# Performance work log

Measured on AMD Instinct MI355X. Metric: run time of the kernel, lower is better.

Reference implementation:

```python
import jax, jax.numpy as jnp
import numpy as np
import math

B, H, S, D = 4, 8, 512, 64

def setup_inputs() -> dict:
    key = jax.random.key(0)
    k1, k2, k3, k4, k5 = jax.random.split(key, 5)
    return {
        "query": jax.random.normal(k1, (B, H, S, D), dtype=jnp.float32),
        "key": jax.random.normal(k2, (B, H, S, D), dtype=jnp.float32),
        "value": jax.random.normal(k3, (B, H, S, D), dtype=jnp.float32),
        "relem": jax.random.normal(k4, (B, S, S, D), dtype=jnp.float32),
        "mask": jax.random.randint(k5, (B, S), 0, 2, dtype=jnp.int32),
    }

def reference(query, key, value, relem, mask):
    d = query.shape[-1]
    # relscore[b,h,s,t] = sum_d q[b,h,s,d] * relem[b,s,t,d]
    relscore = jnp.einsum("bhsd,bstd->bhst", query, relem)
    scores = jnp.einsum("bhsd,bhtd->bhst", query, key)
    scores = (relscore + scores) / math.sqrt(d)
    # mask [B,S] -> [B,1,S,S] (broadcast of key mask over query positions)
    m = mask[:, None, None, :]  # repeat over query dim is a broadcast
    scores = jnp.where(m == 0, jnp.float32(-1e9), scores)
    p_attn = jax.nn.softmax(scores, axis=-1)
    ans1 = jnp.einsum("bhst,bhtd->bhsd", p_attn, value)
    ans2 = jnp.einsum("bhst,bstd->bhsd", p_attn, relem)
    return ans1 + ans2, p_attn
```

## Files before the change

### kernel.cpp

```cpp
#include <hip/hip_runtime.h>


typedef __attribute__((ext_vector_type(8))) short short8;
typedef __attribute__((ext_vector_type(4))) float f32x4;

#define MFMA16(a, b, c) __builtin_amdgcn_mfma_f32_16x16x32_bf16(a, b, c, 0, 0, 0)

__device__ __forceinline__ unsigned short f2bf(float x) {
  unsigned int u = __float_as_uint(x);
  u += 0x7fffu + ((u >> 16) & 1u);
  return (unsigned short)(u >> 16);
}
__device__ __forceinline__ float bf2f(unsigned int s) {
  return __uint_as_float(s << 16);
}
__device__ __forceinline__ short8 pack8(const float4& a, const float4& b) {
  short8 r;
  r[0] = (short)f2bf(a.x); r[1] = (short)f2bf(a.y);
  r[2] = (short)f2bf(a.z); r[3] = (short)f2bf(a.w);
  r[4] = (short)f2bf(b.x); r[5] = (short)f2bf(b.y);
  r[6] = (short)f2bf(b.z); r[7] = (short)f2bf(b.w);
  return r;
}
__device__ __forceinline__ int RLI(int t, int d) {
  return ((t << 6) | d) ^ ((((t & 7) ^ ((t >> 3) & 7))) << 3);
}
__device__ __forceinline__ int SBI(int h, int t) {
  return ((h << 9) | t) ^ ((h & 7) << 3);
}

template <bool WSK>
__global__ __launch_bounds__(256, 4)
void qk_mfma(const float* __restrict__ Q, const float* __restrict__ K,
             void* __restrict__ skout) {
  const int bh   = blockIdx.x >> 6;
  const int tile = blockIdx.x & 63;
  const int s0 = (tile >> 3) << 6;
  const int t0 = (tile & 7) << 6;
  const int w    = threadIdx.x >> 6;
  const int lane = threadIdx.x & 63;
  const int rrow = lane & 15;
  const int kg   = lane >> 4;

  const float* Qb = Q + ((size_t)bh << 15);
  const float* Kb = K + ((size_t)bh << 15);

  const float* qp = Qb + (((s0 + (w << 4) + rrow) << 6) + (kg << 3));
  const short8 a0 = pack8(*reinterpret_cast<const float4*>(qp),
                          *reinterpret_cast<const float4*>(qp + 4));
  const short8 a1 = pack8(*reinterpret_cast<const float4*>(qp + 32),
                          *reinterpret_cast<const float4*>(qp + 36));

  float4 b0, b1, b2, b3;
  {
    const float* kp = Kb + (((t0 + rrow) << 6) + (kg << 3));
    b0 = *reinterpret_cast<const float4*>(kp);
    b1 = *reinterpret_cast<const float4*>(kp + 4);
    b2 = *reinterpret_cast<const float4*>(kp + 32);
    b3 = *reinterpret_cast<const float4*>(kp + 36);
  }
#pragma unroll
  for (int nt = 0; nt < 4; ++nt) {
    const short8 bb0 = pack8(b0, b1);
    const short8 bb1 = pack8(b2, b3);
    if (nt < 3) {
      const float* kp = Kb + (((t0 + ((nt + 1) << 4) + rrow) << 6) + (kg << 3));
      b0 = *reinterpret_cast<const float4*>(kp);
      b1 = *reinterpret_cast<const float4*>(kp + 4);
      b2 = *reinterpret_cast<const float4*>(kp + 32);
      b3 = *reinterpret_cast<const float4*>(kp + 36);
    }
    f32x4 c = {0.0f, 0.0f, 0.0f, 0.0f};
    c = MFMA16(a0, bb0, c);
    c = MFMA16(a1, bb1, c);
    const int tcol = t0 + (nt << 4) + rrow;
    const int srow = s0 + (w << 4) + (kg << 2);
    if constexpr (WSK) {
      unsigned short* ob = (unsigned short*)skout + ((size_t)bh << 18);
#pragma unroll
      for (int r = 0; r < 4; ++r)
        ob[(size_t)(srow + r) * 512 + tcol] = f2bf(c[r]);
    } else {
      float* ob = (float*)skout + ((size_t)bh << 18);
#pragma unroll
      for (int r = 0; r < 4; ++r)
        ob[(size_t)(srow + r) * 512 + tcol] = c[r];
    }
  }
}

template <bool WSK>
__global__ __launch_bounds__(512, 4)
void attn_v8(const float* __restrict__ Q, const float* __restrict__ R,
             const int* __restrict__ Mk, float* __restrict__ ans,
             float* __restrict__ pout, const void* __restrict__ skin) {
  __shared__ __align__(16) unsigned short smem[8 * 512 + 512 * 64];
  __shared__ __align__(16) float Pp[4][8][16];
  unsigned short* Sb = smem;
  unsigned short* Rl = smem + 8 * 512;

  const int tid = threadIdx.x;
  const int b = blockIdx.x >> 9;
  const int s = blockIdx.x & 511;
  const int bh0 = b << 3;

  const float* Rg = R + ((size_t)((b << 9) + s) << 15);

  {
    const int d4 = tid & 15;
    const int tr = tid >> 4;
#pragma unroll
    for (int pg = 0; pg < 2; ++pg) {
      float4 tmp[8];
#pragma unroll
      for (int j = 0; j < 8; ++j) {
        const int t = (pg << 8) + (j << 5) + tr;
        tmp[j] = *reinterpret_cast<const float4*>(Rg + (t << 6) + (d4 << 2));
      }
#pragma unroll
      for (int j = 0; j < 8; ++j) {
        const int t = (pg << 8) + (j << 5) + tr;
        unsigned short* dst = &Rl[RLI(t, d4 << 2)];
        dst[0] = f2bf(tmp[j].x); dst[1] = f2bf(tmp[j].y);
        dst[2] = f2bf(tmp[j].z); dst[3] = f2bf(tmp[j].w);
      }
    }
  }
  __syncthreads();

  const int lane = tid & 63;
  const int w    = tid >> 6;
  const int nn   = lane & 15;
  const int kg   = lane >> 4;

  {
    const int hq = nn & 7;
    const float* Qg = Q + ((size_t)(((bh0 + hq) << 9) + s) << 6);
    const short8 aq0 = pack8(*reinterpret_cast<const float4*>(Qg + (kg << 3)),
                             *reinterpret_cast<const float4*>(Qg + (kg << 3) + 4));
    const short8 aq1 = pack8(*reinterpret_cast<const float4*>(Qg + 32 + (kg << 3)),
                             *reinterpret_cast<const float4*>(Qg + 36 + (kg << 3)));

#pragma unroll
    for (int i = 0; i < 4; ++i) {
      const int t0 = ((w << 2) + i) << 4;
      const short8 bb0 = *reinterpret_cast<const short8*>(&Rl[RLI(t0 + nn, kg << 3)]);
      const short8 bb1 = *reinterpret_cast<const short8*>(&Rl[RLI(t0 + nn, 32 + (kg << 3))]);
      f32x4 c = {0.0f, 0.0f, 0.0f, 0.0f};
      c = MFMA16(aq0, bb0, c);
      c = MFMA16(aq1, bb1, c);
      if (kg < 2) {
#pragma unroll
        for (int r = 0; r < 4; ++r)
          Sb[SBI((kg << 2) + r, t0 + nn)] = f2bf(c[r]);
      }
    }
  }
  __syncthreads();

  {
    const int h = w;
    float bias[8];
#pragma unroll
    for (int k = 0; k < 8; ++k)
      bias[k] = Mk[(b << 9) + lane + (k << 6)] ? 0.0f : -1.0e9f;

    float* po = pout + ((size_t)(bh0 + h) << 18) + ((size_t)s << 9);
    const unsigned short* skw =
        WSK ? (const unsigned short*)skin + ((size_t)(bh0 + h) << 18) + ((size_t)s << 9)
            : nullptr;
    const float* skf =
        WSK ? nullptr
            : (const float*)skin + ((size_t)(bh0 + h) << 18) + ((size_t)s << 9);

    float v[8];
#pragma unroll
    for (int k = 0; k < 8; ++k) {
      const int t = lane + (k << 6);
      const float skv = WSK ? bf2f((unsigned int)skw[t]) : skf[t];
      v[k] = (bf2f((unsigned int)Sb[SBI(h, t)]) + skv) * 0.125f + bias[k];
    }
    float m = v[0];
#pragma unroll
    for (int k = 1; k < 8; ++k) m = fmaxf(m, v[k]);
    m = fmaxf(m, __shfl_xor(m, 1));
    m = fmaxf(m, __shfl_xor(m, 2));
    m = fmaxf(m, __shfl_xor(m, 4));
    m = fmaxf(m, __shfl_xor(m, 8));
    m = fmaxf(m, __shfl_xor(m, 16));
    m = fmaxf(m, __shfl_xor(m, 32));

    float e[8], ss = 0.0f;
#pragma unroll
    for (int k = 0; k < 8; ++k) { e[k] = __expf(v[k] - m); ss += e[k]; }
    ss += __shfl_xor(ss, 1);
    ss += __shfl_xor(ss, 2);
    ss += __shfl_xor(ss, 4);
    ss += __shfl_xor(ss, 8);
    ss += __shfl_xor(ss, 16);
    ss += __shfl_xor(ss, 32);
    const float inv = 1.0f / ss;

#pragma unroll
    for (int k = 0; k < 8; ++k) {
      const float p = e[k] * inv;
      const int t = lane + (k << 6);
      po[t] = p;
      Sb[SBI(h, t)] = f2bf(p);
    }
  }
  __syncthreads();

  {
    const int dt = w & 3;
    const int kh = w >> 2;
    const int n0 = dt << 4;

    f32x4 acc = {0.0f, 0.0f, 0.0f, 0.0f};
#pragma unroll
    for (int k8 = 0; k8 < 8; ++k8) {
      const int tb = (((kh << 3) + k8) << 5) + (kg << 3);
      const short8 af = *reinterpret_cast<const short8*>(&Sb[SBI(nn, tb)]);
      short8 bf;
#pragma unroll
      for (int j = 0; j < 8; ++j)
        bf[j] = (short)Rl[RLI(tb + j, n0 + nn)];
      acc = MFMA16(af, bf, acc);
    }
    if (kh == 1 && kg < 2) {
#pragma unroll
      for (int r = 0; r < 4; ++r)
        Pp[dt][(kg << 2) + r][nn] = acc[r];
    }
    __syncthreads();
    if (kh == 0 && kg < 2) {
#pragma unroll
      for (int r = 0; r < 4; ++r) {
        const int h = (kg << 2) + r;
        ans[((size_t)(((bh0 + h) << 9) + s) << 6) + n0 + nn] =
            acc[r] + Pp[dt][h][nn];
      }
    }
  }
}

__global__ __launch_bounds__(512, 4)
void pv_mfma(const float* __restrict__ V, const float* __restrict__ pout,
             float* __restrict__ ans) {
  __shared__ __align__(16) unsigned short Vl[512 * 64];

  const int tid = threadIdx.x;
  const int bh = blockIdx.x >> 4;
  const int s0 = (blockIdx.x & 15) << 5;

  const float* Vg = V + ((size_t)bh << 15);
  {
    const int d4 = tid & 15;
    const int tr = tid >> 4;
#pragma unroll
    for (int pg = 0; pg < 2; ++pg) {
      float4 tmp[8];
#pragma unroll
      for (int j = 0; j < 8; ++j) {
        const int t = (pg << 8) + (j << 5) + tr;
        tmp[j] = *reinterpret_cast<const float4*>(Vg + (t << 6) + (d4 << 2));
      }
#pragma unroll
      for (int j = 0; j < 8; ++j) {
        const int t = (pg << 8) + (j << 5) + tr;
        unsigned short* dst = &Vl[RLI(t, d4 << 2)];
        dst[0] = f2bf(tmp[j].x); dst[1] = f2bf(tmp[j].y);
        dst[2] = f2bf(tmp[j].z); dst[3] = f2bf(tmp[j].w);
      }
    }
  }
  __syncthreads();

  const int lane = tid & 63;
  const int w    = tid >> 6;
  const int nn   = lane & 15;
  const int kg   = lane >> 4;
  const int rw   = w & 1;
  const int cq   = w >> 1;
  const int n0   = cq << 4;
  const int srow = s0 + (rw << 4) + nn;

  const float* Pg = pout + ((size_t)bh << 18) + ((size_t)srow << 9);

  f32x4 acc = {0.f, 0.f, 0.f, 0.f};

  float4 pa = *reinterpret_cast<const float4*>(Pg + (kg << 3));
  float4 pb = *reinterpret_cast<const float4*>(Pg + (kg << 3) + 4);
#pragma unroll
  for (int ks = 0; ks < 16; ++ks) {
    const short8 af = pack8(pa, pb);
    if (ks < 15) {
      pa = *reinterpret_cast<const float4*>(Pg + ((ks + 1) << 5) + (kg << 3));
      pb = *reinterpret_cast<const float4*>(Pg + ((ks + 1) << 5) + (kg << 3) + 4);
    }
    const int tb = (ks << 5) + (kg << 3);
    short8 bf;
#pragma unroll
    for (int j = 0; j < 8; ++j)
      bf[j] = (short)Vl[RLI(tb + j, n0 + nn)];
    acc = MFMA16(af, bf, acc);
  }

  {
    const int sb = s0 + (rw << 4) + (kg << 2);
#pragma unroll
    for (int r = 0; r < 4; ++r) {
      float* ap = ans + ((size_t)bh << 15) + ((size_t)(sb + r) << 6) + n0 + nn;
      ap[0] += acc[r];
    }
  }
}

extern "C" void kernel_launch(void* const* d_in, const int* in_sizes, int n_in,
                              void* d_out, int out_size, void* d_ws, size_t ws_size,
                              hipStream_t stream) {
  const float* Q  = (const float*)d_in[0];
  const float* K  = (const float*)d_in[1];
  const float* V  = (const float*)d_in[2];
  const float* R  = (const float*)d_in[3];
  const int*   Mk = (const int*)d_in[4];
  float* ans  = (float*)d_out;
  float* pout = ans + (size_t)4 * 8 * 512 * 64;
  (void)in_sizes; (void)n_in; (void)out_size;

  const size_t sk_bf16_bytes = (size_t)4 * 8 * 512 * 512 * 2;

  if (ws_size >= sk_bf16_bytes) {
    hipLaunchKernelGGL((qk_mfma<true>), dim3(2048), dim3(256), 0, stream,
                       Q, K, d_ws);
    hipLaunchKernelGGL((attn_v8<true>), dim3(2048), dim3(512), 0, stream,
                       Q, R, Mk, ans, pout, d_ws);
  } else {
    hipLaunchKernelGGL((qk_mfma<false>), dim3(2048), dim3(256), 0, stream,
                       Q, K, pout);
    hipLaunchKernelGGL((attn_v8<false>), dim3(2048), dim3(512), 0, stream,
                       Q, R, Mk, ans, pout, pout);
  }
  hipLaunchKernelGGL(pv_mfma, dim3(512), dim3(512), 0, stream, V, pout, ans);
}
```

Before: 111.5 us.

## Pipeline relem staging with relscore MFMA and store QK scores as bf16 in pout

The relem tile load is split into two halves. The second half's global loads are issued before the first half's relscore MFMAs and converted into LDS afterwards, so load latency overlaps compute. The QK scores kernel now always writes bf16 values into the first half of each pout float row instead of into workspace, and attn_v10 prefetches those scores and the mask into registers before the relscore phase. This removes the workspace and fallback branch but adds an extra barrier and relies on each block reading its score row before it overwrites pout.

After: 106.1 us. -4.9%, faster.

```diff
diff --git a/kernel.cpp b/kernel.cpp
--- a/kernel.cpp
+++ b/kernel.cpp
@@ -29,10 +29,9 @@
   return ((h << 9) | t) ^ ((h & 7) << 3);
 }
 
-template <bool WSK>
 __global__ __launch_bounds__(256, 4)
 void qk_mfma(const float* __restrict__ Q, const float* __restrict__ K,
-             void* __restrict__ skout) {
+             float* __restrict__ pout) {
   const int bh   = blockIdx.x >> 6;
   const int tile = blockIdx.x & 63;
   const int s0 = (tile >> 3) << 6;
@@ -50,6 +49,8 @@
                           *reinterpret_cast<const float4*>(qp + 4));
   const short8 a1 = pack8(*reinterpret_cast<const float4*>(qp + 32),
                           *reinterpret_cast<const float4*>(qp + 36));
+
+  float* pb = pout + ((size_t)bh << 18);
 
   float4 b0, b1, b2, b3;
   {
@@ -75,25 +76,19 @@
     c = MFMA16(a1, bb1, c);
     const int tcol = t0 + (nt << 4) + rrow;
     const int srow = s0 + (w << 4) + (kg << 2);
-    if constexpr (WSK) {
-      unsigned short* ob = (unsigned short*)skout + ((size_t)bh << 18);
-#pragma unroll
-      for (int r = 0; r < 4; ++r)
-        ob[(size_t)(srow + r) * 512 + tcol] = f2bf(c[r]);
-    } else {
-      float* ob = (float*)skout + ((size_t)bh << 18);
-#pragma unroll
-      for (int r = 0; r < 4; ++r)
-        ob[(size_t)(srow + r) * 512 + tcol] = c[r];
-    }
-  }
-}
-
-template <bool WSK>
+#pragma unroll
+    for (int r = 0; r < 4; ++r) {
+      unsigned short* ob =
+          reinterpret_cast<unsigned short*>(pb + ((size_t)(srow + r) << 9));
+      ob[tcol] = f2bf(c[r]);
+    }
+  }
+}
+
 __global__ __launch_bounds__(512, 4)
-void attn_v8(const float* __restrict__ Q, const float* __restrict__ R,
-             const int* __restrict__ Mk, float* __restrict__ ans,
-             float* __restrict__ pout, const void* __restrict__ skin) {
+void attn_v10(const float* __restrict__ Q, const float* __restrict__ R,
+              const int* __restrict__ Mk, float* __restrict__ ans,
+              float* __restrict__ pout) {
   __shared__ __align__(16) unsigned short smem[8 * 512 + 512 * 64];
   __shared__ __align__(16) float Pp[4][8][16];
   unsigned short* Sb = smem;
@@ -106,26 +101,25 @@
 
   const float* Rg = R + ((size_t)((b << 9) + s) << 15);
 
-  {
-    const int d4 = tid & 15;
-    const int tr = tid >> 4;
-#pragma unroll
-    for (int pg = 0; pg < 2; ++pg) {
-      float4 tmp[8];
-#pragma unroll
-      for (int j = 0; j < 8; ++j) {
-        const int t = (pg << 8) + (j << 5) + tr;
-        tmp[j] = *reinterpret_cast<const float4*>(Rg + (t << 6) + (d4 << 2));
-      }
-#pragma unroll
-      for (int j = 0; j < 8; ++j) {
-        const int t = (pg << 8) + (j << 5) + tr;
-        unsigned short* dst = &Rl[RLI(t, d4 << 2)];
-        dst[0] = f2bf(tmp[j].x); dst[1] = f2bf(tmp[j].y);
-        dst[2] = f2bf(tmp[j].z); dst[3] = f2bf(tmp[j].w);
-      }
-    }
-  }
+  const int d4 = tid & 15;
+  const int tr = tid >> 4;
+
+  float4 buf[8];
+#pragma unroll
+  for (int j = 0; j < 8; ++j)
+    buf[j] = *reinterpret_cast<const float4*>(
+        Rg + (((j << 5) + tr) << 6) + (d4 << 2));
+#pragma unroll
+  for (int j = 0; j < 8; ++j) {
+    const int t = (j << 5) + tr;
+    unsigned short* dst = &Rl[RLI(t, d4 << 2)];
+    dst[0] = f2bf(buf[j].x); dst[1] = f2bf(buf[j].y);
+    dst[2] = f2bf(buf[j].z); dst[3] = f2bf(buf[j].w);
+  }
+#pragma unroll
+  for (int j = 0; j < 8; ++j)
+    buf[j] = *reinterpret_cast<const float4*>(
+        Rg + ((256 + (j << 5) + tr) << 6) + (d4 << 2));
   __syncthreads();
 
   const int lane = tid & 63;
@@ -133,52 +127,71 @@
   const int nn   = lane & 15;
   const int kg   = lane >> 4;
 
-  {
-    const int hq = nn & 7;
-    const float* Qg = Q + ((size_t)(((bh0 + hq) << 9) + s) << 6);
-    const short8 aq0 = pack8(*reinterpret_cast<const float4*>(Qg + (kg << 3)),
-                             *reinterpret_cast<const float4*>(Qg + (kg << 3) + 4));
-    const short8 aq1 = pack8(*reinterpret_cast<const float4*>(Qg + 32 + (kg << 3)),
-                             *reinterpret_cast<const float4*>(Qg + 36 + (kg << 3)));
-
-#pragma unroll
-    for (int i = 0; i < 4; ++i) {
-      const int t0 = ((w << 2) + i) << 4;
-      const short8 bb0 = *reinterpret_cast<const short8*>(&Rl[RLI(t0 + nn, kg << 3)]);
-      const short8 bb1 = *reinterpret_cast<const short8*>(&Rl[RLI(t0 + nn, 32 + (kg << 3))]);
-      f32x4 c = {0.0f, 0.0f, 0.0f, 0.0f};
-      c = MFMA16(aq0, bb0, c);
-      c = MFMA16(aq1, bb1, c);
-      if (kg < 2) {
-#pragma unroll
-        for (int r = 0; r < 4; ++r)
-          Sb[SBI((kg << 2) + r, t0 + nn)] = f2bf(c[r]);
-      }
+  float* po = pout + ((size_t)(bh0 + w) << 18) + ((size_t)s << 9);
+  const unsigned short* skw = reinterpret_cast<const unsigned short*>(po);
+  unsigned int skv[8];
+  int mkv[8];
+#pragma unroll
+  for (int k = 0; k < 8; ++k) {
+    skv[k] = skw[lane + (k << 6)];
+    mkv[k] = Mk[(b << 9) + lane + (k << 6)];
+  }
+
+  const int hq = nn & 7;
+  const float* Qg = Q + ((size_t)(((bh0 + hq) << 9) + s) << 6);
+  const short8 aq0 = pack8(*reinterpret_cast<const float4*>(Qg + (kg << 3)),
+                           *reinterpret_cast<const float4*>(Qg + (kg << 3) + 4));
+  const short8 aq1 = pack8(*reinterpret_cast<const float4*>(Qg + 32 + (kg << 3)),
+                           *reinterpret_cast<const float4*>(Qg + 36 + (kg << 3)));
+
+#pragma unroll
+  for (int i = 0; i < 2; ++i) {
+    const int t0 = ((w << 1) + i) << 4;
+    const short8 bb0 = *reinterpret_cast<const short8*>(&Rl[RLI(t0 + nn, kg << 3)]);
+    const short8 bb1 = *reinterpret_cast<const short8*>(&Rl[RLI(t0 + nn, 32 + (kg << 3))]);
+    f32x4 c = {0.0f, 0.0f, 0.0f, 0.0f};
+    c = MFMA16(aq0, bb0, c);
+    c = MFMA16(aq1, bb1, c);
+    if (kg < 2) {
+#pragma unroll
+      for (int r = 0; r < 4; ++r)
+        Sb[SBI((kg << 2) + r, t0 + nn)] = f2bf(c[r]);
+    }
+  }
+
+#pragma unroll
+  for (int j = 0; j < 8; ++j) {
+    const int t = 256 + (j << 5) + tr;
+    unsigned short* dst = &Rl[RLI(t, d4 << 2)];
+    dst[0] = f2bf(buf[j].x); dst[1] = f2bf(buf[j].y);
+    dst[2] = f2bf(buf[j].z); dst[3] = f2bf(buf[j].w);
+  }
+  __syncthreads();
+
+#pragma unroll
+  for (int i = 0; i < 2; ++i) {
+    const int t0 = 256 + (((w << 1) + i) << 4);
+    const short8 bb0 = *reinterpret_cast<const short8*>(&Rl[RLI(t0 + nn, kg << 3)]);
+    const short8 bb1 = *reinterpret_cast<const short8*>(&Rl[RLI(t0 + nn, 32 + (kg << 3))]);
+    f32x4 c = {0.0f, 0.0f, 0.0f, 0.0f};
+    c = MFMA16(aq0, bb0, c);
+    c = MFMA16(aq1, bb1, c);
+    if (kg < 2) {
+#pragma unroll
+      for (int r = 0; r < 4; ++r)
+        Sb[SBI((kg << 2) + r, t0 + nn)] = f2bf(c[r]);
     }
   }
   __syncthreads();
 
   {
     const int h = w;
-    float bias[8];
-#pragma unroll
-    for (int k = 0; k < 8; ++k)
-      bias[k] = Mk[(b << 9) + lane + (k << 6)] ? 0.0f : -1.0e9f;
-
-    float* po = pout + ((size_t)(bh0 + h) << 18) + ((size_t)s << 9);
-    const unsigned short* skw =
-        WSK ? (const unsigned short*)skin + ((size_t)(bh0 + h) << 18) + ((size_t)s << 9)
-            : nullptr;
-    const float* skf =
-        WSK ? nullptr
-            : (const float*)skin + ((size_t)(bh0 + h) << 18) + ((size_t)s << 9);
-
     float v[8];
 #pragma unroll
     for (int k = 0; k < 8; ++k) {
       const int t = lane + (k << 6);
-      const float skv = WSK ? bf2f((unsigned int)skw[t]) : skf[t];
-      v[k] = (bf2f((unsigned int)Sb[SBI(h, t)]) + skv) * 0.125f + bias[k];
+      v[k] = (bf2f((unsigned int)Sb[SBI(h, t)]) + bf2f(skv[k])) * 0.125f +
+             (mkv[k] ? 0.0f : -1.0e9f);
     }
     float m = v[0];
 #pragma unroll
@@ -213,7 +226,7 @@
 
   {
     const int dt = w & 3;
-    const int kh = w >> 2;
+    const int kh = (w >> 2) & 1;
     const int n0 = dt << 4;
 
     f32x4 acc = {0.0f, 0.0f, 0.0f, 0.0f};
@@ -326,20 +339,10 @@
   const int*   Mk = (const int*)d_in[4];
   float* ans  = (float*)d_out;
   float* pout = ans + (size_t)4 * 8 * 512 * 64;
-  (void)in_sizes; (void)n_in; (void)out_size;
-
-  const size_t sk_bf16_bytes = (size_t)4 * 8 * 512 * 512 * 2;
-
-  if (ws_size >= sk_bf16_bytes) {
-    hipLaunchKernelGGL((qk_mfma<true>), dim3(2048), dim3(256), 0, stream,
-                       Q, K, d_ws);
-    hipLaunchKernelGGL((attn_v8<true>), dim3(2048), dim3(512), 0, stream,
-                       Q, R, Mk, ans, pout, d_ws);
-  } else {
-    hipLaunchKernelGGL((qk_mfma<false>), dim3(2048), dim3(256), 0, stream,
-                       Q, K, pout);
-    hipLaunchKernelGGL((attn_v8<false>), dim3(2048), dim3(512), 0, stream,
-                       Q, R, Mk, ans, pout, pout);
-  }
+  (void)d_ws; (void)ws_size; (void)in_sizes; (void)n_in; (void)out_size;
+
+  hipLaunchKernelGGL(qk_mfma, dim3(2048), dim3(256), 0, stream, Q, K, pout);
+  hipLaunchKernelGGL(attn_v10, dim3(2048), dim3(512), 0, stream,
+                     Q, R, Mk, ans, pout);
   hipLaunchKernelGGL(pv_mfma, dim3(512), dim3(512), 0, stream, V, pout, ans);
 }
```
